# Kernel optimization log

Measured on AMD Instinct MI355X. Metric: run time of the kernel, lower is better.

Reference implementation:

```python
import jax, jax.numpy as jnp
import numpy as np

NUM_HEADS = 16
EMB_DIM = 1024
IN_CH = 512
D_CTX = 768
DEPTH = EMB_DIM // NUM_HEADS
SCALE = DEPTH ** -0.5
NEG = -1e9


def setup_inputs() -> dict:
    key = jax.random.key(0)
    ks = jax.random.split(key, 12)
    B, N, S = 4, 4096, 256
    def lin(kw, fan_in, fan_out):
        lim = 1.0 / np.sqrt(fan_in)
        w = jax.random.uniform(kw, (fan_out, fan_in), jnp.float32, -lim, lim)
        return w
    return {
        'x': jax.random.normal(ks[0], (B, N, IN_CH), jnp.float32),
        'context': jax.random.normal(ks[1], (B, S, D_CTX), jnp.float32),
        'pad_mask': jnp.ones((B, N), jnp.float32),
        'seq_mask': jnp.ones((B, S), jnp.float32),
        'Wq_w': lin(ks[2], IN_CH, EMB_DIM), 'Wq_b': jnp.zeros((EMB_DIM,), jnp.float32),
        'Wk_w': lin(ks[3], D_CTX, EMB_DIM), 'Wk_b': jnp.zeros((EMB_DIM,), jnp.float32),
        'Wv_w': lin(ks[4], D_CTX, EMB_DIM), 'Wv_b': jnp.zeros((EMB_DIM,), jnp.float32),
        'P1_w': lin(ks[5], EMB_DIM, EMB_DIM), 'P1_b': jnp.zeros((EMB_DIM,), jnp.float32),
        'P2_w': lin(ks[6], EMB_DIM, IN_CH), 'P2_b': jnp.zeros((IN_CH,), jnp.float32),
    }


def reference(x, context, pad_mask, seq_mask, Wq_w, Wq_b, Wk_w, Wk_b, Wv_w, Wv_b, P1_w, P1_b, P2_w, P2_b):
    B, N, _ = x.shape
    S = context.shape[1]
    # QKV projections, split into heads: [B, H, N|S, D]
    Q = (x @ Wq_w.T + Wq_b).reshape(B, N, NUM_HEADS, DEPTH).transpose(0, 2, 1, 3)
    K = (context @ Wk_w.T + Wk_b).reshape(B, S, NUM_HEADS, DEPTH).transpose(0, 2, 1, 3)
    V = (context @ Wv_w.T + Wv_b).reshape(B, S, NUM_HEADS, DEPTH).transpose(0, 2, 1, 3)
    # attention scores [B, H, N, S]
    att = jnp.einsum('bnid,bnjd->bnij', Q, K) * SCALE
    # outer-product mask: pad_mask[B,N] x seq_mask[B,S] -> [B,1,N,S]
    mask = (pad_mask[:, :, None] * seq_mask[:, None, :])[:, None, :, :]
    att = jnp.where(mask != 0.0, att, NEG)
    att = jax.nn.softmax(att, axis=-1)
    out = jnp.einsum('bnij,bnjd->bnid', att, V)
    out = out.transpose(0, 2, 1, 3).reshape(B, N, EMB_DIM)
    # proj_out MLP: Linear -> ReLU -> Linear
    out = jax.nn.relu(out @ P1_w.T + P1_b) @ P2_w.T + P2_b
    return out
```

## Files before the change

### kernel.cpp

```cpp
#include <hip/hip_runtime.h>
#include <hip/hip_bf16.h>
#include <stdint.h>

typedef __attribute__((ext_vector_type(8))) short bf16x8;
typedef __attribute__((ext_vector_type(4))) short s16x4;
typedef __attribute__((ext_vector_type(4))) float f32x4;

#define MFMA16(a, b, c) __builtin_amdgcn_mfma_f32_16x16x32_bf16((a), (b), (c), 0, 0, 0)
#define MFMAH(a, b, c) __builtin_amdgcn_mfma_f32_16x16x16bf16_1k((a), (b), (c), 0, 0, 0)

__device__ __forceinline__ void gload_lds16(const void* g, void* l) {
  __builtin_amdgcn_global_load_lds((const __attribute__((address_space(1))) void*)g,
                                   (__attribute__((address_space(3))) void*)l, 16, 0, 0);
}

__global__ void cvt_all(const float* __restrict__ s0, const float* __restrict__ s1,
                        const float* __restrict__ s2, const float* __restrict__ s3,
                        const float* __restrict__ s4, const float* __restrict__ s5,
                        const float* __restrict__ s6,
                        __hip_bfloat16* __restrict__ d0, __hip_bfloat16* __restrict__ d1,
                        __hip_bfloat16* __restrict__ d2, __hip_bfloat16* __restrict__ d3,
                        __hip_bfloat16* __restrict__ d4, __hip_bfloat16* __restrict__ d5,
                        __hip_bfloat16* __restrict__ d6) {
  constexpr int e0 = 2097152;
  constexpr int e1 = e0 + 196608;
  constexpr int e2 = e1 + 131072;
  constexpr int e3 = e2 + 196608;
  constexpr int e4 = e3 + 196608;
  constexpr int e5 = e4 + 262144;
  constexpr int e6 = e5 + 131072;
  const int stride = gridDim.x * blockDim.x;
  for (int i = blockIdx.x * blockDim.x + threadIdx.x; i < e6; i += stride) {
    const float* s; __hip_bfloat16* d; int j;
    if (i < e0)      { s = s0; d = d0; j = i; }
    else if (i < e1) { s = s1; d = d1; j = i - e0; }
    else if (i < e2) { s = s2; d = d2; j = i - e1; }
    else if (i < e3) { s = s3; d = d3; j = i - e2; }
    else if (i < e4) { s = s4; d = d4; j = i - e3; }
    else if (i < e5) { s = s5; d = d5; j = i - e4; }
    else             { s = s6; d = d6; j = i - e5; }
    const float4 v = *(const float4*)(s + (size_t)j * 4);
    s16x4 o;
    __hip_bfloat16 h;
    h = __float2bfloat16(v.x); o[0] = *(short*)&h;
    h = __float2bfloat16(v.y); o[1] = *(short*)&h;
    h = __float2bfloat16(v.z); o[2] = *(short*)&h;
    h = __float2bfloat16(v.w); o[3] = *(short*)&h;
    *(s16x4*)((short*)d + (size_t)j * 4) = o;
  }
}


template <int RELU, int OUTMODE>
__global__ __launch_bounds__(256, 2) void gemm_bt(
    const __hip_bfloat16* __restrict__ Abf, const __hip_bfloat16* __restrict__ Wbf,
    const float* __restrict__ bias, void* __restrict__ Cv,
    int M, int N, int K) {
  __shared__ __align__(16) __hip_bfloat16 As[128 * 32];
  __shared__ __align__(16) __hip_bfloat16 Bs[128 * 32];
  const int t = threadIdx.x;
  const int w = t >> 6, lane = t & 63;
  const int lr = lane & 15, lg = lane >> 4;
  const int m0 = blockIdx.x * 128, n0 = blockIdx.y * 128;
  const int wr = (w >> 1) * 64, wc = (w & 1) * 64;

  const char* Ag = (const char*)Abf;
  const char* Wg = (const char*)Wbf;
  const size_t ldb = (size_t)K * 2;

  f32x4 acc[4][4] = {};

  const int o0 = (w << 10) + lane * 16;
  const int o1 = o0 + 4096;
  const int r0 = o0 >> 6, gc0 = ((((o0 >> 4) & 3) ^ ((r0 >> 1) & 3)) << 4);
  const int r1 = o1 >> 6, gc1 = ((((o1 >> 4) & 3) ^ ((r1 >> 1) & 3)) << 4);
  const int slx = (lg ^ ((lr >> 1) & 3)) << 4;

  for (int kt = 0; kt < K; kt += 32) {
    if (kt) __syncthreads();
    gload_lds16(Ag + (size_t)(m0 + r0) * ldb + kt * 2 + gc0, (char*)As + (w << 10));
    gload_lds16(Ag + (size_t)(m0 + r1) * ldb + kt * 2 + gc1, (char*)As + 4096 + (w << 10));
    gload_lds16(Wg + (size_t)(n0 + r0) * ldb + kt * 2 + gc0, (char*)Bs + (w << 10));
    gload_lds16(Wg + (size_t)(n0 + r1) * ldb + kt * 2 + gc1, (char*)Bs + 4096 + (w << 10));
    __syncthreads();

    bf16x8 af[4], bfv[4];
#pragma unroll
    for (int mi = 0; mi < 4; ++mi)
      af[mi] = *(const bf16x8*)((const char*)As + ((wr + mi * 16 + lr) << 6) + slx);
#pragma unroll
    for (int ni = 0; ni < 4; ++ni)
      bfv[ni] = *(const bf16x8*)((const char*)Bs + ((wc + ni * 16 + lr) << 6) + slx);
#pragma unroll
    for (int mi = 0; mi < 4; ++mi)
#pragma unroll
      for (int ni = 0; ni < 4; ++ni)
        acc[mi][ni] = MFMA16(af[mi], bfv[ni], acc[mi][ni]);
  }

#pragma unroll
  for (int ni = 0; ni < 4; ++ni) {
    const int col = n0 + wc + ni * 16 + lr;
    const float bv = bias[col];
#pragma unroll
    for (int mi = 0; mi < 4; ++mi) {
      const int row = m0 + wr + mi * 16 + lg * 4;
#pragma unroll
      for (int j = 0; j < 4; ++j) {
        float v = acc[mi][ni][j] + bv;
        if (RELU) v = fmaxf(v, 0.0f);
        if (OUTMODE == 0) {
          ((__hip_bfloat16*)Cv)[(size_t)(row + j) * N + col] = __float2bfloat16(v);
        } else if (OUTMODE == 1) {
          ((float*)Cv)[(size_t)(row + j) * N + col] = v;
        } else {
          const int rb = (row + j) >> 8, s = (row + j) & 255;
          const int hh = col >> 6, d = col & 63;
          ((__hip_bfloat16*)Cv)[(((size_t)(rb * 16 + hh) * 64 + d) << 8) + s] =
              __float2bfloat16(v);
        }
      }
    }
  }
}

__device__ __forceinline__ void gemm128_lite(
    const __hip_bfloat16* __restrict__ Abf, const __hip_bfloat16* __restrict__ Wbf,
    const float* __restrict__ bias, __hip_bfloat16* __restrict__ C,
    int N, int K, int outmode, int relu, int bx, int by) {
  __shared__ __align__(16) __hip_bfloat16 AsL[2][128 * 32];
  __shared__ __align__(16) __hip_bfloat16 BsL[2][256 * 32];
  const int t = threadIdx.x;
  const int w = t >> 6, lane = t & 63;
  const int lr = lane & 15, lg = lane >> 4;
  const int m0 = bx * 128, n0 = by * 256;
  const int wr = (w >> 2) * 64, wc = (w & 3) * 64;

  const char* Ag = (const char*)Abf;
  const char* Wg = (const char*)Wbf;
  const size_t ldb = (size_t)K * 2;

  f32x4 acc[4][4] = {};

  const int o0 = (w << 10) + lane * 16;
  const int o1 = o0 + 8192;
  const int r0 = o0 >> 6, gc0 = ((((o0 >> 4) & 3) ^ ((r0 >> 1) & 3)) << 4);
  const int r1 = o1 >> 6, gc1 = ((((o1 >> 4) & 3) ^ ((r1 >> 1) & 3)) << 4);
  const int slx = (lg ^ ((lr >> 1) & 3)) << 4;
  const int db0 = (w << 10);
  const int db1 = 8192 + (w << 10);

  auto STAGE_A = [&](int buf, int tile) {
    const int kt = tile << 5;
    gload_lds16(Ag + (size_t)(m0 + r0) * ldb + kt * 2 + gc0, (char*)AsL[buf] + db0);
  };
  auto STAGE_B = [&](int buf, int tile) {
    const int kt = tile << 5;
    gload_lds16(Wg + (size_t)(n0 + r0) * ldb + kt * 2 + gc0, (char*)BsL[buf] + db0);
    gload_lds16(Wg + (size_t)(n0 + r1) * ldb + kt * 2 + gc1, (char*)BsL[buf] + db1);
  };

  const int nt = K >> 5;
  STAGE_A(0, 0); STAGE_B(0, 0);
  asm volatile("s_waitcnt vmcnt(0)" ::: "memory");
  asm volatile("s_barrier" ::: "memory");
  for (int j = 0; j < nt; ++j) {
    const int buf = j & 1;
    const int stage = (j + 1 < nt);
    bf16x8 af0[2], af1[2], bfv[4];
#pragma unroll
    for (int mi = 0; mi < 2; ++mi)
      af0[mi] = *(const bf16x8*)((const char*)AsL[buf] + ((wr + mi * 16 + lr) << 6) + slx);
#pragma unroll
    for (int ni = 0; ni < 4; ++ni)
      bfv[ni] = *(const bf16x8*)((const char*)BsL[buf] + ((wc + ni * 16 + lr) << 6) + slx);
    if (stage) STAGE_A(buf ^ 1, j + 1);
    asm volatile("s_barrier" ::: "memory");
    asm volatile("s_waitcnt lgkmcnt(0)" ::: "memory");
    __builtin_amdgcn_sched_barrier(0);
    __builtin_amdgcn_s_setprio(1);
#pragma unroll
    for (int mi = 0; mi < 2; ++mi)
#pragma unroll
      for (int ni = 0; ni < 4; ++ni)
        acc[mi][ni] = MFMA16(af0[mi], bfv[ni], acc[mi][ni]);
    __builtin_amdgcn_s_setprio(0);
    asm volatile("s_barrier" ::: "memory");
#pragma unroll
    for (int mi = 0; mi < 2; ++mi)
      af1[mi] = *(const bf16x8*)((const char*)AsL[buf] + ((wr + (mi + 2) * 16 + lr) << 6) + slx);
    if (stage) STAGE_B(buf ^ 1, j + 1);
    asm volatile("s_barrier" ::: "memory");
    asm volatile("s_waitcnt lgkmcnt(0)" ::: "memory");
    __builtin_amdgcn_sched_barrier(0);
    __builtin_amdgcn_s_setprio(1);
#pragma unroll
    for (int mi = 0; mi < 2; ++mi)
#pragma unroll
      for (int ni = 0; ni < 4; ++ni)
        acc[mi + 2][ni] = MFMA16(af1[mi], bfv[ni], acc[mi + 2][ni]);
    __builtin_amdgcn_s_setprio(0);
    if (stage) asm volatile("s_waitcnt vmcnt(0)" ::: "memory");
    asm volatile("s_barrier" ::: "memory");
  }

#pragma unroll
  for (int ni = 0; ni < 4; ++ni) {
    const int col = n0 + wc + ni * 16 + lr;
    const float bv = bias[col];
#pragma unroll
    for (int mi = 0; mi < 4; ++mi) {
      const int row = m0 + wr + mi * 16 + lg * 4;
#pragma unroll
      for (int j = 0; j < 4; ++j) {
        float v = acc[mi][ni][j] + bv;
        if (relu) v = fmaxf(v, 0.0f);
        if (outmode == 0) {
          C[(size_t)(row + j) * N + col] = __float2bfloat16(v);
        } else {
          const int rb = (row + j) >> 8, s = (row + j) & 255;
          const int hh = col >> 6, d = col & 63;
          C[(((size_t)(rb * 16 + hh) * 64 + d) << 8) + s] = __float2bfloat16(v);
        }
      }
    }
  }
}

__global__ __launch_bounds__(512, 4) void gemm256_qkv(
    const __hip_bfloat16* __restrict__ xb, const __hip_bfloat16* __restrict__ ctxb,
    const __hip_bfloat16* __restrict__ Wq, const __hip_bfloat16* __restrict__ Wk,
    const __hip_bfloat16* __restrict__ Wv,
    const float* __restrict__ bq, const float* __restrict__ bk, const float* __restrict__ bv,
    __hip_bfloat16* __restrict__ Q, __hip_bfloat16* __restrict__ Kp,
    __hip_bfloat16* __restrict__ Vt) {
  const int bid = blockIdx.x;
  if (bid < 32) {
    gemm128_lite(ctxb, Wk, bk, Kp, 1024, 768, 0, 0, bid >> 2, bid & 3);
  } else if (bid < 64) {
    const int l = bid - 32;
    gemm128_lite(ctxb, Wv, bv, Vt, 1024, 768, 2, 0, l >> 2, l & 3);
  } else {
    const int l = bid - 64;
    const int rb = (l & 7) * 64 + (l >> 3);
    gemm128_lite(xb, Wq, bq, Q, 1024, 512, 0, 0, rb >> 2, rb & 3);
  }
}

__global__ __launch_bounds__(512, 4) void gemm256_p1(
    const __hip_bfloat16* __restrict__ A, const __hip_bfloat16* __restrict__ W,
    const float* __restrict__ bias, __hip_bfloat16* __restrict__ C) {
  const int l = blockIdx.x;
  const int rb = (l & 7) * 64 + (l >> 3);
  gemm128_lite(A, W, bias, C, 1024, 1024, 0, 1, rb >> 2, rb & 3);
}

__global__ __launch_bounds__(512, 4) void attn_fused(
    const __hip_bfloat16* __restrict__ Qb, const __hip_bfloat16* __restrict__ Kb,
    const __hip_bfloat16* __restrict__ Vtg, const float* __restrict__ padm,
    const float* __restrict__ seqm, __hip_bfloat16* __restrict__ O) {
  constexpr int S = 256, E = 1024, Nq = 4096;
  constexpr float NEGV = -1e9f;
  __shared__ __align__(16) char smem[65536];
  char* VtB = smem;
  char* KsB = smem + 32768;

  const int t = threadIdx.x;
  const int w = t >> 6, lane = t & 63;
  const int lr = lane & 15, lg = lane >> 4;
  const int h = blockIdx.y, b = blockIdx.z;

  const char* Kg = (const char*)(Kb + (size_t)b * S * E + h * 64);
#pragma unroll
  for (int i = 0; i < 4; ++i) {
    const int o = ((i * 8 + w) << 10) + lane * 16;
    const int s = o >> 7, bc = o & 127;
    gload_lds16(Kg + (size_t)s * (E * 2) + (bc ^ ((s & 7) << 4)), KsB + ((i * 8 + w) << 10));
  }
  const char* Vg = (const char*)Vtg + ((size_t)(b * 16 + h) << 15);
#pragma unroll
  for (int i = 0; i < 4; ++i) {
    const int o = ((i * 8 + w) << 10) + lane * 16;
    const int d = o >> 9, c = o & 511;
    gload_lds16(Vg + (d << 9) + (c ^ ((d & 7) << 4)), VtB + ((i * 8 + w) << 10));
  }

  const int qw = blockIdx.x * 128 + w * 16;
  const short* Qg = (const short*)Qb + (size_t)(b * Nq + qw + lr) * E + h * 64;
  const bf16x8 aq0 = *(const bf16x8*)(Qg + (lg << 3));
  const bf16x8 aq1 = *(const bf16x8*)(Qg + 32 + (lg << 3));
  const float padq = padm[(size_t)b * Nq + qw + lr];
  const float qbias = (padq != 0.f) ? 0.f : NEGV;

  __syncthreads();

  const int swz = (lr & 7) << 4;
  f32x4 o[4] = {};
  float ssum = 0.f;
#pragma unroll
  for (int ni = 0; ni < 16; ++ni) {
    const int s = ni * 16 + lr;
    const bf16x8 bk0 = *(const bf16x8*)(KsB + (s << 7) + ((lg << 4) ^ swz));
    const bf16x8 bk1 = *(const bf16x8*)(KsB + (s << 7) + ((64 + (lg << 4)) ^ swz));
    f32x4 a = {};
    a = MFMA16(bk0, aq0, a);
    a = MFMA16(bk1, aq1, a);

    const float4 sm4 = *(const float4*)(seqm + (size_t)b * S + ni * 16 + lg * 4);
    const float e0 = __expf(a[0] * 0.125f + ((sm4.x != 0.f ? 0.f : NEGV) + qbias));
    const float e1 = __expf(a[1] * 0.125f + ((sm4.y != 0.f ? 0.f : NEGV) + qbias));
    const float e2 = __expf(a[2] * 0.125f + ((sm4.z != 0.f ? 0.f : NEGV) + qbias));
    const float e3 = __expf(a[3] * 0.125f + ((sm4.w != 0.f ? 0.f : NEGV) + qbias));
    ssum += (e0 + e1) + (e2 + e3);

    s16x4 pf;
    __hip_bfloat16 hh;
    hh = __float2bfloat16(e0); pf[0] = *(short*)&hh;
    hh = __float2bfloat16(e1); pf[1] = *(short*)&hh;
    hh = __float2bfloat16(e2); pf[2] = *(short*)&hh;
    hh = __float2bfloat16(e3); pf[3] = *(short*)&hh;

    const int sb = (ni * 32 + lg * 8);
#pragma unroll
    for (int nd = 0; nd < 4; ++nd) {
      const int d = nd * 16 + lr;
      const s16x4 bv = *(const s16x4*)(VtB + (d << 9) + (sb ^ swz));
      o[nd] = MFMAH(pf, bv, o[nd]);
    }
  }

  ssum += __shfl_xor(ssum, 16);
  ssum += __shfl_xor(ssum, 32);
  const float inv = 1.0f / ssum;
  float invj[4];
#pragma unroll
  for (int j = 0; j < 4; ++j) invj[j] = __shfl(inv, lg * 4 + j);

  __hip_bfloat16* Og = O + (size_t)(b * Nq + qw) * E + h * 64;
#pragma unroll
  for (int nd = 0; nd < 4; ++nd)
#pragma unroll
    for (int j = 0; j < 4; ++j)
      Og[(size_t)(lg * 4 + j) * E + nd * 16 + lr] = __float2bfloat16(o[nd][j] * invj[j]);
}

extern "C" void kernel_launch(void* const* d_in, const int* in_sizes, int n_in,
                              void* d_out, int out_size, void* d_ws, size_t ws_size,
                              hipStream_t stream) {
  const float* x    = (const float*)d_in[0];
  const float* ctx  = (const float*)d_in[1];
  const float* padm = (const float*)d_in[2];
  const float* seqm = (const float*)d_in[3];
  const float* Wq_w = (const float*)d_in[4];
  const float* Wq_b = (const float*)d_in[5];
  const float* Wk_w = (const float*)d_in[6];
  const float* Wk_b = (const float*)d_in[7];
  const float* Wv_w = (const float*)d_in[8];
  const float* Wv_b = (const float*)d_in[9];
  const float* P1_w = (const float*)d_in[10];
  const float* P1_b = (const float*)d_in[11];
  const float* P2_w = (const float*)d_in[12];
  const float* P2_b = (const float*)d_in[13];
  float* out = (float*)d_out;

  char* ws = (char*)d_ws;
  size_t off = 0;
  auto alloc = [&](size_t bytes) { char* p = ws + off; off += (bytes + 255) & ~(size_t)255; return p; };
  __hip_bfloat16* Q    = (__hip_bfloat16*)alloc(16384ull * 1024 * 2);
  __hip_bfloat16* AO   = (__hip_bfloat16*)alloc(16384ull * 1024 * 2);
  __hip_bfloat16* xb   = (__hip_bfloat16*)alloc(16384ull * 512 * 2);
  __hip_bfloat16* ctxb = (__hip_bfloat16*)alloc(1024ull * 768 * 2);
  __hip_bfloat16* Kp   = (__hip_bfloat16*)alloc(1024ull * 1024 * 2);
  __hip_bfloat16* Vt   = (__hip_bfloat16*)alloc(1024ull * 1024 * 2);
  __hip_bfloat16* Wqb  = (__hip_bfloat16*)alloc(1024ull * 512 * 2);
  __hip_bfloat16* Wkb  = (__hip_bfloat16*)alloc(1024ull * 768 * 2);
  __hip_bfloat16* Wvb  = (__hip_bfloat16*)alloc(1024ull * 768 * 2);
  __hip_bfloat16* P1b  = (__hip_bfloat16*)alloc(1024ull * 1024 * 2);
  __hip_bfloat16* P2b  = (__hip_bfloat16*)alloc(512ull * 1024 * 2);
  __hip_bfloat16* O1   = Q;

  cvt_all<<<dim3(2048, 1, 1), dim3(256, 1, 1), 0, stream>>>(
      x, ctx, Wq_w, Wk_w, Wv_w, P1_w, P2_w, xb, ctxb, Wqb, Wkb, Wvb, P1b, P2b);

  gemm256_qkv<<<dim3(576, 1, 1), dim3(512, 1, 1), 0, stream>>>(
      xb, ctxb, Wqb, Wkb, Wvb, Wq_b, Wk_b, Wv_b, Q, Kp, Vt);
  attn_fused<<<dim3(32, 16, 4), dim3(512, 1, 1), 0, stream>>>(Q, Kp, Vt, padm, seqm, AO);
  gemm256_p1<<<dim3(512, 1, 1), dim3(512, 1, 1), 0, stream>>>(AO, P1b, P1_b, O1);
  gemm_bt<0, 1><<<dim3(128, 4, 1), dim3(256, 1, 1), 0, stream>>>(O1, P2b, P2_b, out, 16384, 512, 1024);
}
```

Measured before the change: 156.3 us.

## Route P2 projection through pipelined 128x256 GEMM and streamline softmax exp

The final 1024->512 projection moves off the simple single-buffered 128x128 GEMM and onto the double-buffered, 512-thread gemm128_lite path. That path gains an fp32 output mode and uses a remapped block order, which should improve load/compute overlap and L2 reuse. In the attention kernel, the softmax exponent now uses exp2f with the log2(e) factor folded into the scale constant. Masking becomes a fused multiply-add on the mask values instead of compare-and-select, which cuts per-element ALU work. That masking assumes masks are exactly 0 or 1, unlike the reference's nonzero test.

```diff
diff --git a/kernel.cpp b/kernel.cpp
--- a/kernel.cpp
+++ b/kernel.cpp
@@ -51,82 +51,9 @@
 }
 
 
-template <int RELU, int OUTMODE>
-__global__ __launch_bounds__(256, 2) void gemm_bt(
+__device__ __forceinline__ void gemm128_lite(
     const __hip_bfloat16* __restrict__ Abf, const __hip_bfloat16* __restrict__ Wbf,
     const float* __restrict__ bias, void* __restrict__ Cv,
-    int M, int N, int K) {
-  __shared__ __align__(16) __hip_bfloat16 As[128 * 32];
-  __shared__ __align__(16) __hip_bfloat16 Bs[128 * 32];
-  const int t = threadIdx.x;
-  const int w = t >> 6, lane = t & 63;
-  const int lr = lane & 15, lg = lane >> 4;
-  const int m0 = blockIdx.x * 128, n0 = blockIdx.y * 128;
-  const int wr = (w >> 1) * 64, wc = (w & 1) * 64;
-
-  const char* Ag = (const char*)Abf;
-  const char* Wg = (const char*)Wbf;
-  const size_t ldb = (size_t)K * 2;
-
-  f32x4 acc[4][4] = {};
-
-  const int o0 = (w << 10) + lane * 16;
-  const int o1 = o0 + 4096;
-  const int r0 = o0 >> 6, gc0 = ((((o0 >> 4) & 3) ^ ((r0 >> 1) & 3)) << 4);
-  const int r1 = o1 >> 6, gc1 = ((((o1 >> 4) & 3) ^ ((r1 >> 1) & 3)) << 4);
-  const int slx = (lg ^ ((lr >> 1) & 3)) << 4;
-
-  for (int kt = 0; kt < K; kt += 32) {
-    if (kt) __syncthreads();
-    gload_lds16(Ag + (size_t)(m0 + r0) * ldb + kt * 2 + gc0, (char*)As + (w << 10));
-    gload_lds16(Ag + (size_t)(m0 + r1) * ldb + kt * 2 + gc1, (char*)As + 4096 + (w << 10));
-    gload_lds16(Wg + (size_t)(n0 + r0) * ldb + kt * 2 + gc0, (char*)Bs + (w << 10));
-    gload_lds16(Wg + (size_t)(n0 + r1) * ldb + kt * 2 + gc1, (char*)Bs + 4096 + (w << 10));
-    __syncthreads();
-
-    bf16x8 af[4], bfv[4];
-#pragma unroll
-    for (int mi = 0; mi < 4; ++mi)
-      af[mi] = *(const bf16x8*)((const char*)As + ((wr + mi * 16 + lr) << 6) + slx);
-#pragma unroll
-    for (int ni = 0; ni < 4; ++ni)
-      bfv[ni] = *(const bf16x8*)((const char*)Bs + ((wc + ni * 16 + lr) << 6) + slx);
-#pragma unroll
-    for (int mi = 0; mi < 4; ++mi)
-#pragma unroll
-      for (int ni = 0; ni < 4; ++ni)
-        acc[mi][ni] = MFMA16(af[mi], bfv[ni], acc[mi][ni]);
-  }
-
-#pragma unroll
-  for (int ni = 0; ni < 4; ++ni) {
-    const int col = n0 + wc + ni * 16 + lr;
-    const float bv = bias[col];
-#pragma unroll
-    for (int mi = 0; mi < 4; ++mi) {
-      const int row = m0 + wr + mi * 16 + lg * 4;
-#pragma unroll
-      for (int j = 0; j < 4; ++j) {
-        float v = acc[mi][ni][j] + bv;
-        if (RELU) v = fmaxf(v, 0.0f);
-        if (OUTMODE == 0) {
-          ((__hip_bfloat16*)Cv)[(size_t)(row + j) * N + col] = __float2bfloat16(v);
-        } else if (OUTMODE == 1) {
-          ((float*)Cv)[(size_t)(row + j) * N + col] = v;
-        } else {
-          const int rb = (row + j) >> 8, s = (row + j) & 255;
-          const int hh = col >> 6, d = col & 63;
-          ((__hip_bfloat16*)Cv)[(((size_t)(rb * 16 + hh) * 64 + d) << 8) + s] =
-              __float2bfloat16(v);
-        }
-      }
-    }
-  }
-}
-
-__device__ __forceinline__ void gemm128_lite(
-    const __hip_bfloat16* __restrict__ Abf, const __hip_bfloat16* __restrict__ Wbf,
-    const float* __restrict__ bias, __hip_bfloat16* __restrict__ C,
     int N, int K, int outmode, int relu, int bx, int by) {
   __shared__ __align__(16) __hip_bfloat16 AsL[2][128 * 32];
   __shared__ __align__(16) __hip_bfloat16 BsL[2][256 * 32];
@@ -216,11 +143,14 @@
         float v = acc[mi][ni][j] + bv;
         if (relu) v = fmaxf(v, 0.0f);
         if (outmode == 0) {
-          C[(size_t)(row + j) * N + col] = __float2bfloat16(v);
+          ((__hip_bfloat16*)Cv)[(size_t)(row + j) * N + col] = __float2bfloat16(v);
+        } else if (outmode == 1) {
+          ((float*)Cv)[(size_t)(row + j) * N + col] = v;
         } else {
           const int rb = (row + j) >> 8, s = (row + j) & 255;
           const int hh = col >> 6, d = col & 63;
-          C[(((size_t)(rb * 16 + hh) * 64 + d) << 8) + s] = __float2bfloat16(v);
+          ((__hip_bfloat16*)Cv)[(((size_t)(rb * 16 + hh) * 64 + d) << 8) + s] =
+              __float2bfloat16(v);
         }
       }
     }
@@ -255,12 +185,21 @@
   gemm128_lite(A, W, bias, C, 1024, 1024, 0, 1, rb >> 2, rb & 3);
 }
 
+__global__ __launch_bounds__(512, 4) void gemm256_p2(
+    const __hip_bfloat16* __restrict__ A, const __hip_bfloat16* __restrict__ W,
+    const float* __restrict__ bias, float* __restrict__ C) {
+  const int l = blockIdx.x;
+  const int rb = (l & 7) * 32 + (l >> 3);
+  gemm128_lite(A, W, bias, C, 512, 1024, 1, 0, rb >> 1, rb & 1);
+}
+
 __global__ __launch_bounds__(512, 4) void attn_fused(
     const __hip_bfloat16* __restrict__ Qb, const __hip_bfloat16* __restrict__ Kb,
     const __hip_bfloat16* __restrict__ Vtg, const float* __restrict__ padm,
     const float* __restrict__ seqm, __hip_bfloat16* __restrict__ O) {
   constexpr int S = 256, E = 1024, Nq = 4096;
-  constexpr float NEGV = -1e9f;
+  constexpr float BIG = 1e9f;
+  constexpr float C1 = 0.125f * 1.44269504088896f;
   __shared__ __align__(16) char smem[65536];
   char* VtB = smem;
   char* KsB = smem + 32768;
@@ -290,7 +229,7 @@
   const bf16x8 aq0 = *(const bf16x8*)(Qg + (lg << 3));
   const bf16x8 aq1 = *(const bf16x8*)(Qg + 32 + (lg << 3));
   const float padq = padm[(size_t)b * Nq + qw + lr];
-  const float qbias = (padq != 0.f) ? 0.f : NEGV;
+  const float pB = padq * BIG;
 
   __syncthreads();
 
@@ -307,10 +246,10 @@
     a = MFMA16(bk1, aq1, a);
 
     const float4 sm4 = *(const float4*)(seqm + (size_t)b * S + ni * 16 + lg * 4);
-    const float e0 = __expf(a[0] * 0.125f + ((sm4.x != 0.f ? 0.f : NEGV) + qbias));
-    const float e1 = __expf(a[1] * 0.125f + ((sm4.y != 0.f ? 0.f : NEGV) + qbias));
-    const float e2 = __expf(a[2] * 0.125f + ((sm4.z != 0.f ? 0.f : NEGV) + qbias));
-    const float e3 = __expf(a[3] * 0.125f + ((sm4.w != 0.f ? 0.f : NEGV) + qbias));
+    const float e0 = exp2f(fmaf(a[0], C1, fmaf(sm4.x, pB, -BIG)));
+    const float e1 = exp2f(fmaf(a[1], C1, fmaf(sm4.y, pB, -BIG)));
+    const float e2 = exp2f(fmaf(a[2], C1, fmaf(sm4.z, pB, -BIG)));
+    const float e3 = exp2f(fmaf(a[3], C1, fmaf(sm4.w, pB, -BIG)));
     ssum += (e0 + e1) + (e2 + e3);
 
     s16x4 pf;
@@ -386,5 +325,5 @@
       xb, ctxb, Wqb, Wkb, Wvb, Wq_b, Wk_b, Wv_b, Q, Kp, Vt);
   attn_fused<<<dim3(32, 16, 4), dim3(512, 1, 1), 0, stream>>>(Q, Kp, Vt, padm, seqm, AO);
   gemm256_p1<<<dim3(512, 1, 1), dim3(512, 1, 1), 0, stream>>>(AO, P1b, P1_b, O1);
-  gemm_bt<0, 1><<<dim3(128, 4, 1), dim3(256, 1, 1), 0, stream>>>(O1, P2b, P2_b, out, 16384, 512, 1024);
-}
+  gemm256_p2<<<dim3(256, 1, 1), dim3(512, 1, 1), 0, stream>>>(O1, P2b, P2_b, out);
+}
```

Measured after the change: 160.2 us. 1.02x slower.
